# Performance work log

Measured on AMD Instinct MI355X. Metric: run time of the kernel, lower is better.

The kernel has to match this reference:

```python
import jax, jax.numpy as jnp
import numpy as np

B, C, H, W = 2, 256, 64, 64
HEADS, SR = 8, 4
D = C // HEADS          # head dim = 32
N = H * W               # query length = 4096
EPS = 1e-5


def _conv(x, w, stride=1, pad=0, groups=1, b=None):
    out = jax.lax.conv_general_dilated(
        x, w, (stride, stride), [(pad, pad), (pad, pad)],
        dimension_numbers=('NCHW', 'OIHW', 'NCHW'),
        feature_group_count=groups)
    if b is not None:
        out = out + b[None, :, None, None]
    return out


def _bn(x, p):
    # p: [4, C] = (gamma, beta, running_mean, running_var), eval-mode BN
    g, b, m, v = p[0], p[1], p[2], p[3]
    s = g / jnp.sqrt(v + EPS)
    return (x - m[None, :, None, None]) * s[None, :, None, None] + b[None, :, None, None]


def setup_inputs() -> dict:
    key = jax.random.key(0)
    ks = iter(jax.random.split(key, 32))
    nrm = lambda shape, s=0.05: jax.random.normal(next(ks), shape, jnp.float32) * s
    def bnp():
        return jnp.stack([jnp.ones((C,), jnp.float32), jnp.zeros((C,), jnp.float32),
                          jax.random.normal(next(ks), (C,), jnp.float32) * 0.1,
                          jax.random.uniform(next(ks), (C,), jnp.float32) + 0.5])
    return dict(
        x=jax.random.normal(next(ks), (B, C, H, W), jnp.float32),
        relative_pos_enc=jax.random.normal(next(ks), (B, 2, 64, 64), jnp.float32),
        q_w=nrm((C, C, 1, 1)), q_b=jnp.zeros((C,), jnp.float32),
        kv_w=nrm((2 * C, C, 1, 1)), kv_b=jnp.zeros((2 * C,), jnp.float32),
        sr1_dw_w=nrm((C, 1, SR + 3, SR + 3)), sr1_bn1=bnp(),
        sr1_pw_w=nrm((C, 1, 1, 1), 0.5), sr1_bn2=bnp(),
        sr2_dw_w=nrm((C, 1, SR // 2 + 3, SR // 2 + 3)), sr2_bn1=bnp(),
        sr2_pw_w=nrm((C, 1, 1, 1), 0.5), sr2_bn2=bnp(),
        local_w=nrm((C, 1, 3, 3)), local_b=jnp.zeros((C,), jnp.float32),
    )


def reference(x, relative_pos_enc, q_w, q_b, kv_w, kv_b,
              sr1_dw_w, sr1_bn1, sr1_pw_w, sr1_bn2,
              sr2_dw_w, sr2_bn1, sr2_pw_w, sr2_bn2,
              local_w, local_b):
    scale = D ** -0.5
    # q: 1x1 conv -> [B, heads, N, D]; both branches use the FIRST half of heads
    q = _conv(x, q_w, b=q_b).reshape(B, HEADS, D, N).transpose(0, 1, 3, 2)
    qh = q[:, :HEADS // 2]

    def branch(dw_w, bn1, pw_w, bn2, stride, pad, rpe_slice):
        # SR path: depthwise conv + BN + ReLU, depthwise 1x1 + BN
        y = jax.nn.relu(_bn(_conv(x, dw_w, stride, pad, groups=C), bn1))
        y = _bn(_conv(y, pw_w, groups=C), bn2)
        # local 3x3 depthwise mixing with residual
        y = _conv(y, local_w, pad=1, groups=C, b=local_b) + y
        kv = _conv(y, kv_w, b=kv_b)                # [B, 2C, h', w']
        k, v = jnp.split(kv, 2, axis=1)
        L = 2 * y.shape[2] * y.shape[3]            # channel-fold doubles kv length
        k = k.reshape(B, HEADS // 2, D, L)
        v = v.reshape(B, HEADS // 2, D, L).transpose(0, 1, 3, 2)
        attn = jnp.einsum('bhnd,bhdl->bhnl', qh, k) * scale
        rpe = jax.image.resize(rpe_slice, (B, 1, N, L), method='bicubic')
        attn = jax.nn.softmax(attn + rpe, axis=-1)
        return jnp.einsum('bhnl,bhld->bhnd', attn, v)

    x1 = branch(sr1_dw_w, sr1_bn1, sr1_pw_w, sr1_bn2,
                SR, (SR + 3) // 2, relative_pos_enc[:, 0:1])
    x2 = branch(sr2_dw_w, sr2_bn1, sr2_pw_w, sr2_bn2,
                SR // 2, (SR // 2 + 3) // 2, relative_pos_enc[:, 1:2])
    out = jnp.concatenate([x1, x2], axis=-1)       # [B, heads//2, N, 2D]
    return out.reshape(B, C, H, W)
```

## Files before the change

kernel.cpp:

```cpp
#include <hip/hip_runtime.h>
#include <hip/hip_bf16.h>
#include <math.h>

#define NB 2
#define NC 256
#define HWIN 4096
#define NN 4096
#define ND 32
#define NHH 4
#define EPSV 1e-5f

typedef short short8 __attribute__((ext_vector_type(8)));
typedef float f32x4 __attribute__((ext_vector_type(4)));
typedef unsigned short u16;
typedef unsigned int u32;

#define OFF_T1   0
#define OFF_T2   262144
#define OFF_Q    1310720
#define OFF_KT1  1835008
#define OFF_VT1  1900544
#define OFF_KT2  1966080
#define OFF_VT2  2228224
#define OFF_RCT1 2490368
#define OFF_RCT2 2531328
#define OFF_WT   2695168
#define OFF_QWT  5054464
#define OFF_LWP  5087232

#define QSCALE 0.2550437314857726f
#define LOG2E  1.4426950408889634f

__device__ __forceinline__ u16 f2bf(float x) {
  unsigned u = __float_as_uint(x);
  u += 0x7fffu + ((u >> 16) & 1u);
  return (u16)(u >> 16);
}

__device__ __forceinline__ u32 pk_bf16(float a, float b) {
  __hip_bfloat162 h = __float22bfloat162_rn(make_float2(a, b));
  u32 r; __builtin_memcpy(&r, &h, 4);
  return r;
}

__device__ __forceinline__ float keysw(float t) {
  t = fabsf(t);
  float w;
  if (t < 1.f)       w = ((1.5f*t - 2.5f)*t)*t + 1.f;
  else if (t < 2.f)  w = ((-0.5f*t + 2.5f)*t - 4.f)*t + 2.f;
  else               w = 0.f;
  return w;
}

template<int KS, int STR, int PAD, int OH>
__device__ __forceinline__ void dwconv_body(int idx, const float* __restrict__ x,
    const float* __restrict__ dww, const float* __restrict__ bn1,
    const float* __restrict__ pww, const float* __restrict__ bn2,
    float* __restrict__ tout) {
  const int hw = OH*OH;
  int s = idx % hw; int c = (idx/hw) % NC; int b = idx/(hw*NC);
  int oy = s / OH, ox = s % OH;
  const float* xp = x + (b*NC + c)*HWIN;
  const float* wp = dww + c*KS*KS;
  float acc = 0.f;
  #pragma unroll
  for (int ky = 0; ky < KS; ++ky) {
    int iy = oy*STR - PAD + ky;
    if (iy < 0 || iy >= 64) continue;
    #pragma unroll
    for (int kx = 0; kx < KS; ++kx) {
      int ix = ox*STR - PAD + kx;
      if (ix < 0 || ix >= 64) continue;
      acc += xp[iy*64 + ix] * wp[ky*KS + kx];
    }
  }
  float s1 = bn1[c] * rsqrtf(bn1[3*NC + c] + EPSV);
  float z = (acc - bn1[2*NC + c])*s1 + bn1[NC + c];
  z = fmaxf(z, 0.f);
  float s2 = bn2[c] * rsqrtf(bn2[3*NC + c] + EPSV);
  z = z * (pww[c]*s2) + (bn2[NC + c] - bn2[2*NC + c]*s2);
  tout[((size_t)(b*hw + s))*NC + c] = z;
}

__device__ __forceinline__ void rpe_body(int idx, const float* __restrict__ rpe,
                                         u16* __restrict__ rcT, int L, int ch) {
  int r = idx & 63; int l = (idx >> 6) % L; int b = idx / (64*L);
  float f = ((float)l + 0.5f)*(64.f/(float)L) - 0.5f;
  int i0 = (int)floorf(f) - 1;
  const float* rp = rpe + ((b*2 + ch)*64 + r)*64;
  float v = 0.f, wsum = 0.f;
  #pragma unroll
  for (int j = 0; j < 4; ++j) {
    int i = i0 + j;
    if (i >= 0 && i < 64) {
      float w = keysw(f - (float)i);
      v += w * rp[i]; wsum += w;
    }
  }
  rcT[((size_t)(b*L + l))*80 + 4 + r] = f2bf(v / wsum);
}

__global__ void __launch_bounds__(256) prep_kernel(
    const float* __restrict__ x,
    const float* __restrict__ dw1, const float* __restrict__ bn11,
    const float* __restrict__ pw1, const float* __restrict__ bn12, float* __restrict__ t1,
    const float* __restrict__ dw2, const float* __restrict__ bn21,
    const float* __restrict__ pw2, const float* __restrict__ bn22, float* __restrict__ t2,
    const float* __restrict__ rpe, u16* __restrict__ rct1, u16* __restrict__ rct2,
    const float* __restrict__ kvw, float* __restrict__ wtp,
    const float* __restrict__ qw, float* __restrict__ qwp2,
    const float* __restrict__ lw, float* __restrict__ lwp) {
  int blk = blockIdx.x;
  int t = threadIdx.x;
  if (blk < 512) {
    dwconv_body<7,4,3,16>(blk*256 + t, x, dw1, bn11, pw1, bn12, t1);
  } else if (blk < 2560) {
    dwconv_body<5,2,2,32>((blk-512)*256 + t, x, dw2, bn21, pw2, bn22, t2);
  } else if (blk < 2816) {
    rpe_body((blk-2560)*256 + t, rpe, rct1, 512, 0);
  } else if (blk < 3840) {
    rpe_body((blk-2816)*256 + t, rpe, rct2, 2048, 1);
  } else if (blk < 3968) {
    int idx = (blk-3840)*256 + t;
    float4 vv = *(const float4*)(kvw + (size_t)idx*4);
    int o = idx >> 6, c4 = idx & 63;
    *(float4*)(wtp + ((size_t)(c4*512 + o))*4) = vv;
  } else if (blk < 4000) {
    int idx = (blk-3968)*256 + t;
    float4 vv = *(const float4*)(qw + (size_t)idx*4);
    int oc = idx >> 6, c0 = (idx & 63)*4;
    int ocq = oc >> 2, r = oc & 3;
    qwp2[((size_t)((c0+0)*32 + ocq))*4 + r] = vv.x;
    qwp2[((size_t)((c0+1)*32 + ocq))*4 + r] = vv.y;
    qwp2[((size_t)((c0+2)*32 + ocq))*4 + r] = vv.z;
    qwp2[((size_t)((c0+3)*32 + ocq))*4 + r] = vv.w;
  } else {
    int c = t;
    #pragma unroll
    for (int tp = 0; tp < 9; ++tp) lwp[tp*256 + c] = lw[c*9 + tp];
  }
}

__global__ void __launch_bounds__(256) localkv_kernel(
    const float* __restrict__ t1T, const float* __restrict__ t2T,
    const float* __restrict__ lwp, const float* __restrict__ lb,
    const float* __restrict__ wtp, const float* __restrict__ kvb,
    u16* __restrict__ kt1, u16* __restrict__ vt1,
    u16* __restrict__ kt2, u16* __restrict__ vt2,
    const float* __restrict__ x, const float* __restrict__ qwp2,
    const float* __restrict__ qb, u16* __restrict__ q) {
  __shared__ float sbuf[128*32];
  int blk = blockIdx.x, tid = threadIdx.x;
  if (blk < 640) {
    int kv = blk & 1, ti = blk >> 1;
    const float* tT; u16 *kT, *vT; int OH, hw, b, s0;
    if (ti < 64) { tT = t1T; kT = kt1; vT = vt1; OH = 16; hw = 256;  b = ti >> 5; s0 = (ti & 31)*8; }
    else { int v2 = ti-64; tT = t2T; kT = kt2; vT = vt2; OH = 32; hw = 1024; b = v2 >> 7; s0 = (v2 & 127)*8; }
    int oy = s0 / OH, ox0 = s0 % OH;
    const float* tb = tT + (size_t)b*hw*NC;
    int cl = tid & 63, spg = tid >> 6;
    int c0 = cl*4;
    f32x4 wt9[9];
    #pragma unroll
    for (int tp = 0; tp < 9; ++tp) wt9[tp] = *(const f32x4*)(lwp + tp*256 + c0);
    f32x4 lb4 = *(const f32x4*)(lb + c0);
    #pragma unroll
    for (int i = 0; i < 2; ++i) {
      int sp = spg*2 + i;
      int ox = ox0 + sp;
      f32x4 a = lb4;
      #pragma unroll
      for (int dy = 0; dy < 3; ++dy) {
        int iy = oy + dy - 1;
        if (iy < 0 || iy >= OH) continue;
        #pragma unroll
        for (int dx = 0; dx < 3; ++dx) {
          int ix = ox + dx - 1;
          if (ix < 0 || ix >= OH) continue;
          f32x4 tv = *(const f32x4*)(tb + (size_t)(iy*OH + ix)*NC + c0);
          a += tv * wt9[dy*3 + dx];
        }
      }
      a += *(const f32x4*)(tb + (size_t)(oy*OH + ox)*NC + c0);
      *(f32x4*)(sbuf + sp*NC + c0) = a;
    }
    __syncthreads();
    int ol = tid & 127, sph = tid >> 7;
    int o0i = kv*256 + ol, o1i = o0i + 128;
    float acc0[4], acc1[4];
    float b0 = kvb[o0i], b1 = kvb[o1i];
    #pragma unroll
    for (int i = 0; i < 4; ++i) { acc0[i] = b0; acc1[i] = b1; }
    #pragma unroll 2
    for (int c4 = 0; c4 < 64; ++c4) {
      f32x4 w0 = *(const f32x4*)(wtp + ((size_t)(c4*512 + o0i))*4);
      f32x4 w1 = *(const f32x4*)(wtp + ((size_t)(c4*512 + o1i))*4);
      #pragma unroll
      for (int i = 0; i < 4; ++i) {
        f32x4 y4 = *(const f32x4*)(sbuf + (sph*4 + i)*NC + c4*4);
        #pragma unroll
        for (int j = 0; j < 4; ++j) { acc0[i] += w0[j]*y4[j]; acc1[i] += w1[j]*y4[j]; }
      }
    }
    int L2 = 2*hw;
    #pragma unroll
    for (int k = 0; k < 2; ++k) {
      const float* ap = k ? acc1 : acc0;
      int oo = ol + k*128;
      int hh = oo >> 6, r = oo & 63, d = r >> 1, e = r & 1;
      if (kv == 0) {
        u16* kp = kT + ((size_t)((b*NHH + hh)*L2 + e*hw + s0 + sph*4))*ND + d;
        #pragma unroll
        for (int j = 0; j < 4; ++j) kp[j*ND] = f2bf(ap[j]);
      } else {
        int l0v = e*hw + s0 + sph*4;
        u16* vp = vT + ((size_t)((b*NHH + hh)*(L2/64) + (l0v >> 6))*ND + d)*64 + (l0v & 63);
        #pragma unroll
        for (int j = 0; j < 4; ++j) vp[j] = f2bf(ap[j]);
      }
    }
  } else {
    int qblk = blk - 640;
    int b = qblk >> 7;
    int n0 = (qblk & 127) * 32;
    const float* xb = x + (size_t)b*NC*HWIN + n0;
    int ocq = tid & 31, spg = tid >> 5;
    float acc[4][4];
    #pragma unroll
    for (int k = 0; k < 4; ++k) {
      float bias = qb[ocq*4 + k];
      #pragma unroll
      for (int i = 0; i < 4; ++i) acc[k][i] = bias;
    }
    #pragma unroll
    for (int half = 0; half < 2; ++half) {
      #pragma unroll
      for (int j = 0; j < 4; ++j) {
        int u = tid + 256*j;
        int c = u >> 3, spq = u & 7;
        *(f32x4*)(sbuf + c*32 + spq*4) =
            *(const f32x4*)(xb + (size_t)(half*128 + c)*HWIN + spq*4);
      }
      __syncthreads();
      #pragma unroll 4
      for (int c = 0; c < 128; ++c) {
        int cg = half*128 + c;
        f32x4 w4 = *(const f32x4*)(qwp2 + ((size_t)(cg*32 + ocq))*4);
        f32x4 y4 = *(const f32x4*)(sbuf + c*32 + spg*4);
        #pragma unroll
        for (int k = 0; k < 4; ++k)
          #pragma unroll
          for (int i = 0; i < 4; ++i) acc[k][i] += w4[k]*y4[i];
      }
      __syncthreads();
    }
    #pragma unroll
    for (int k = 0; k < 4; ++k) {
      int oc = ocq*4 + k;
      int h = oc >> 5, d = oc & 31;
      u16* qp = q + (((size_t)(b*NHH + h))*NN + n0 + spg*4)*ND + d;
      #pragma unroll
      for (int i = 0; i < 4; ++i) qp[i*ND] = f2bf(acc[k][i]*QSCALE);
    }
  }
}

__global__ void __launch_bounds__(256) attn_kernel(
    const u16* __restrict__ qbf,
    const u16* __restrict__ kt1, const u16* __restrict__ vt1, const u16* __restrict__ rct1,
    const u16* __restrict__ kt2, const u16* __restrict__ vt2, const u16* __restrict__ rct2,
    float* __restrict__ out) {
  __shared__ u16 kbuf[64*32];
  __shared__ u16 vbuf[32*64];
  __shared__ u32 pbuf_all[4][16*32];
  int u = blockIdx.x;
  int br, b, hh, rb;
  if (u < 512) { br = 1; b = u >> 8; hh = (u >> 6) & 3; rb = u & 63; }
  else { int v = u - 512; br = 0; b = v >> 8; hh = (v >> 6) & 3; rb = v & 63; }
  int L = br ? 2048 : 512;
  int nt = br ? 32 : 8;
  const u16* kT  = br ? kt2 : kt1;
  const u16* vT  = br ? vt2 : vt1;
  const u16* rcT = br ? rct2 : rct1;
  int tid = threadIdx.x;
  int w = tid >> 6, lane = tid & 63;
  int g = lane >> 4, lo = lane & 15;
  u32* pbuf = pbuf_all[w];
  u16* pbuf16 = (u16*)pbuf;
  int n = rb*64 + w*16 + lo;

  const u16* kbase = kT + (size_t)(b*NHH + hh)*L*ND;
  const u16* vbase = vT + (size_t)(b*NHH + hh)*ND*L;
  const u16* rcTb  = rcT + (size_t)b*L*80;

  short8 qf = *(const short8*)(qbf + (((size_t)(b*NHH + hh))*NN + n)*ND + 8*g);

  float fr = ((float)n + 0.5f)*(1.f/64.f) - 0.5f;
  int ri0 = (int)floorf(fr) - 1;
  int a = (w < 2) ? rb - 2 : rb - 1;
  int rmin = a & ~3;
  float wr4[4]; float wsum = 0.f;
  #pragma unroll
  for (int j = 0; j < 4; ++j) {
    int i = ri0 + j;
    float wv = (i >= 0 && i < 64) ? keysw(fr - (float)i) : 0.f;
    wr4[j] = wv; wsum += wv;
  }
  float invw = LOG2E / wsum;
  float wt8[8];
  #pragma unroll
  for (int s = 0; s < 8; ++s) {
    float acc = 0.f;
    #pragma unroll
    for (int j = 0; j < 4; ++j)
      acc += (ri0 + j - rmin == s) ? wr4[j]*invw : 0.f;
    wt8[s] = acc;
  }
  short8 wtf;
  {
    u32 p0 = pk_bf16(wt8[0], wt8[1]), p1 = pk_bf16(wt8[2], wt8[3]);
    u32 p2 = pk_bf16(wt8[4], wt8[5]), p3 = pk_bf16(wt8[6], wt8[7]);
    uint4 uu = make_uint4(p0, p1, p2, p3);
    wtf = __builtin_bit_cast(short8, uu);
    if (g != 0) wtf = (short8)0;
  }
  const u16* rcrow0 = rcTb + (rmin + 4);

  const f32x4 zero = {0.f, 0.f, 0.f, 0.f};
  float ssum = 0.f;
  f32x4 o0 = zero, o1 = zero;

  int kr_row = tid >> 2, kr_col = (tid & 3)*8;
  int kr_sw  = ((kr_row >> 1) & 3)*8;
  int vr_row = tid >> 3, vr_col = (tid & 7)*8;
  int vr_sw  = (vr_row & 7)*8;
  int ksw = ((lo >> 1) & 3)*8;
  int vsw = (lo & 7)*8;
  int psw4 = (lo & 7)*4;
  int psw8 = (lo & 7)*8;

  auto stageLoad = [&](short8& kr, short8& vr, int l0) {
    kr = *(const short8*)(kbase + (size_t)(l0 + kr_row)*ND + kr_col);
    vr = *(const short8*)(vbase + (size_t)(l0 >> 6)*(ND*64) + vr_row*64 + vr_col);
  };
  auto stageStore = [&](short8 kr, short8 vr) {
    *(short8*)(kbuf + kr_row*32 + (kr_col ^ kr_sw)) = kr;
    *(short8*)(vbuf + vr_row*64 + (vr_col ^ vr_sw)) = vr;
  };
  auto loadRC = [&](uint4 (&rc)[4], int l0) {
    #pragma unroll
    for (int c = 0; c < 4; ++c) {
      const u16* arow = rcrow0 + (size_t)(l0 + 16*c + lo)*80;
      uint2 ra = *(const uint2*)arow;
      uint2 rb2 = *(const uint2*)(arow + 4);
      rc[c] = make_uint4(ra.x, ra.y, rb2.x, rb2.y);
    }
  };

  short8 kr, vr;
  uint4 rcA[4], rcB[4];
  stageLoad(kr, vr, 0);
  loadRC(rcA, 0);

  for (int t = 0; t < nt; ++t) {
    stageStore(kr, vr);
    __syncthreads();
    if (t < nt-1) { stageLoad(kr, vr, (t+1)*64); loadRC(rcB, (t+1)*64); }
    f32x4 s4[4];
    #pragma unroll
    for (int c = 0; c < 4; ++c) {
      short8 rcf = __builtin_bit_cast(short8, rcA[c]);
      f32x4 accr = __builtin_amdgcn_mfma_f32_16x16x32_bf16(rcf, wtf, zero, 0, 0, 0);
      short8 kf = *(const short8*)(kbuf + (16*c + lo)*32 + ((8*g) ^ ksw));
      s4[c] = __builtin_amdgcn_mfma_f32_16x16x32_bf16(kf, qf, accr, 0, 0, 0);
    }
    float psum = 0.f;
    u32 pk[8];
    #pragma unroll
    for (int c = 0; c < 4; ++c) {
      float p0 = __builtin_amdgcn_exp2f(s4[c][0]);
      float p1 = __builtin_amdgcn_exp2f(s4[c][1]);
      float p2 = __builtin_amdgcn_exp2f(s4[c][2]);
      float p3 = __builtin_amdgcn_exp2f(s4[c][3]);
      psum += (p0 + p1) + (p2 + p3);
      pk[2*c]   = pk_bf16(p0, p1);
      pk[2*c+1] = pk_bf16(p2, p3);
    }
    ssum += psum;
    #pragma unroll
    for (int c = 0; c < 4; ++c)
      *(uint2*)(pbuf + lo*32 + ((8*c + 2*g) ^ psw4)) = make_uint2(pk[2*c], pk[2*c+1]);
    short8 pf0 = *(const short8*)(pbuf16 + lo*64 + ((8*g) ^ psw8));
    short8 pf1 = *(const short8*)(pbuf16 + lo*64 + ((32 + 8*g) ^ psw8));
    short8 v00 = *(const short8*)(vbuf + lo*64 + ((8*g) ^ vsw));
    short8 v01 = *(const short8*)(vbuf + lo*64 + ((32 + 8*g) ^ vsw));
    short8 v10 = *(const short8*)(vbuf + (16 + lo)*64 + ((8*g) ^ vsw));
    short8 v11 = *(const short8*)(vbuf + (16 + lo)*64 + ((32 + 8*g) ^ vsw));
    o0 = __builtin_amdgcn_mfma_f32_16x16x32_bf16(v00, pf0, o0, 0, 0, 0);
    o1 = __builtin_amdgcn_mfma_f32_16x16x32_bf16(v10, pf0, o1, 0, 0, 0);
    o0 = __builtin_amdgcn_mfma_f32_16x16x32_bf16(v01, pf1, o0, 0, 0, 0);
    o1 = __builtin_amdgcn_mfma_f32_16x16x32_bf16(v11, pf1, o1, 0, 0, 0);
    if (t < nt-1) {
      #pragma unroll
      for (int j = 0; j < 4; ++j) rcA[j] = rcB[j];
    }
    __syncthreads();
  }

  ssum += __shfl_xor(ssum, 16, 64);
  ssum += __shfl_xor(ssum, 32, 64);
  float inv = 1.f/ssum;
  f32x4 w0 = o0*inv, w1 = o1*inv;
  float* op = out + ((size_t)((b*NC + hh*64 + rb)*64 + (w*16 + lo)))*64 + (br ? 32 : 0);
  *(f32x4*)(op + 4*g)      = w0;
  *(f32x4*)(op + 16 + 4*g) = w1;
}

extern "C" void kernel_launch(void* const* d_in, const int* in_sizes, int n_in,
                              void* d_out, int out_size, void* d_ws, size_t ws_size,
                              hipStream_t stream) {
  const float* x    = (const float*)d_in[0];
  const float* rpe  = (const float*)d_in[1];
  const float* qw   = (const float*)d_in[2];
  const float* qb   = (const float*)d_in[3];
  const float* kvw  = (const float*)d_in[4];
  const float* kvb  = (const float*)d_in[5];
  const float* dw1  = (const float*)d_in[6];
  const float* bn11 = (const float*)d_in[7];
  const float* pw1  = (const float*)d_in[8];
  const float* bn12 = (const float*)d_in[9];
  const float* dw2  = (const float*)d_in[10];
  const float* bn21 = (const float*)d_in[11];
  const float* pw2  = (const float*)d_in[12];
  const float* bn22 = (const float*)d_in[13];
  const float* lw   = (const float*)d_in[14];
  const float* lb   = (const float*)d_in[15];
  float* out = (float*)d_out;
  float* ws  = (float*)d_ws;

  float* t1   = ws + OFF_T1;
  float* t2   = ws + OFF_T2;
  u16*   q    = (u16*)(ws + OFF_Q);
  u16*   kt1  = (u16*)(ws + OFF_KT1);
  u16*   vt1  = (u16*)(ws + OFF_VT1);
  u16*   kt2  = (u16*)(ws + OFF_KT2);
  u16*   vt2  = (u16*)(ws + OFF_VT2);
  u16*   rct1 = (u16*)(ws + OFF_RCT1);
  u16*   rct2 = (u16*)(ws + OFF_RCT2);
  float* wtp  = ws + OFF_WT;
  float* qwp2 = ws + OFF_QWT;
  float* lwp  = ws + OFF_LWP;

  hipLaunchKernelGGL(prep_kernel, dim3(4001), dim3(256), 0, stream,
                     x, dw1, bn11, pw1, bn12, t1, dw2, bn21, pw2, bn22, t2,
                     rpe, rct1, rct2, kvw, wtp, qw, qwp2, lw, lwp);
  hipLaunchKernelGGL(localkv_kernel, dim3(896), dim3(256), 0, stream,
                     t1, t2, lwp, lb, wtp, kvb, kt1, vt1, kt2, vt2, x, qwp2, qb, q);
  hipLaunchKernelGGL(attn_kernel, dim3(1024), dim3(256), 0, stream,
                     q, kt1, vt1, rct1, kt2, vt2, rct2, out);
}
```

Measured before the change: 171.3 us.

## Merge both attention branches per block and move RPE resize into localkv kernel

The attention kernel now has each block process both branches in sequence (the short L=512 pass, then the L=2048 pass), halving the grid to 512 blocks and reusing the Q fragment and bicubic row weights across the two passes. The RPE bicubic resize work moves from the prep kernel into the localkv kernel as extra blocks, rebalancing work across stages. The intent is to remove the load imbalance between short and long branch blocks and duplicated per-block setup. The risk is fewer blocks in attention, giving lower occupancy and longer serial blocks on a GPU with many CUs.

```diff
diff --git a/kernel.cpp b/kernel.cpp
--- a/kernel.cpp
+++ b/kernel.cpp
@@ -106,7 +106,6 @@
     const float* __restrict__ pw1, const float* __restrict__ bn12, float* __restrict__ t1,
     const float* __restrict__ dw2, const float* __restrict__ bn21,
     const float* __restrict__ pw2, const float* __restrict__ bn22, float* __restrict__ t2,
-    const float* __restrict__ rpe, u16* __restrict__ rct1, u16* __restrict__ rct2,
     const float* __restrict__ kvw, float* __restrict__ wtp,
     const float* __restrict__ qw, float* __restrict__ qwp2,
     const float* __restrict__ lw, float* __restrict__ lwp) {
@@ -116,17 +115,13 @@
     dwconv_body<7,4,3,16>(blk*256 + t, x, dw1, bn11, pw1, bn12, t1);
   } else if (blk < 2560) {
     dwconv_body<5,2,2,32>((blk-512)*256 + t, x, dw2, bn21, pw2, bn22, t2);
-  } else if (blk < 2816) {
-    rpe_body((blk-2560)*256 + t, rpe, rct1, 512, 0);
-  } else if (blk < 3840) {
-    rpe_body((blk-2816)*256 + t, rpe, rct2, 2048, 1);
-  } else if (blk < 3968) {
-    int idx = (blk-3840)*256 + t;
+  } else if (blk < 2688) {
+    int idx = (blk-2560)*256 + t;
     float4 vv = *(const float4*)(kvw + (size_t)idx*4);
     int o = idx >> 6, c4 = idx & 63;
     *(float4*)(wtp + ((size_t)(c4*512 + o))*4) = vv;
-  } else if (blk < 4000) {
-    int idx = (blk-3968)*256 + t;
+  } else if (blk < 2720) {
+    int idx = (blk-2688)*256 + t;
     float4 vv = *(const float4*)(qw + (size_t)idx*4);
     int oc = idx >> 6, c0 = (idx & 63)*4;
     int ocq = oc >> 2, r = oc & 3;
@@ -148,7 +143,8 @@
     u16* __restrict__ kt1, u16* __restrict__ vt1,
     u16* __restrict__ kt2, u16* __restrict__ vt2,
     const float* __restrict__ x, const float* __restrict__ qwp2,
-    const float* __restrict__ qb, u16* __restrict__ q) {
+    const float* __restrict__ qb, u16* __restrict__ q,
+    const float* __restrict__ rpe, u16* __restrict__ rct1, u16* __restrict__ rct2) {
   __shared__ float sbuf[128*32];
   int blk = blockIdx.x, tid = threadIdx.x;
   if (blk < 640) {
@@ -219,7 +215,7 @@
         for (int j = 0; j < 4; ++j) vp[j] = f2bf(ap[j]);
       }
     }
-  } else {
+  } else if (blk < 896) {
     int qblk = blk - 640;
     int b = qblk >> 7;
     int n0 = (qblk & 127) * 32;
@@ -262,6 +258,10 @@
       #pragma unroll
       for (int i = 0; i < 4; ++i) qp[i*ND] = f2bf(acc[k][i]*QSCALE);
     }
+  } else if (blk < 1152) {
+    rpe_body((blk-896)*256 + tid, rpe, rct1, 512, 0);
+  } else {
+    rpe_body((blk-1152)*256 + tid, rpe, rct2, 2048, 1);
   }
 }
 
@@ -274,24 +274,13 @@
   __shared__ u16 vbuf[32*64];
   __shared__ u32 pbuf_all[4][16*32];
   int u = blockIdx.x;
-  int br, b, hh, rb;
-  if (u < 512) { br = 1; b = u >> 8; hh = (u >> 6) & 3; rb = u & 63; }
-  else { int v = u - 512; br = 0; b = v >> 8; hh = (v >> 6) & 3; rb = v & 63; }
-  int L = br ? 2048 : 512;
-  int nt = br ? 32 : 8;
-  const u16* kT  = br ? kt2 : kt1;
-  const u16* vT  = br ? vt2 : vt1;
-  const u16* rcT = br ? rct2 : rct1;
+  int b = u >> 8, hh = (u >> 6) & 3, rb = u & 63;
   int tid = threadIdx.x;
   int w = tid >> 6, lane = tid & 63;
   int g = lane >> 4, lo = lane & 15;
   u32* pbuf = pbuf_all[w];
   u16* pbuf16 = (u16*)pbuf;
   int n = rb*64 + w*16 + lo;
-
-  const u16* kbase = kT + (size_t)(b*NHH + hh)*L*ND;
-  const u16* vbase = vT + (size_t)(b*NHH + hh)*ND*L;
-  const u16* rcTb  = rcT + (size_t)b*L*80;
 
   short8 qf = *(const short8*)(qbf + (((size_t)(b*NHH + hh))*NN + n)*ND + 8*g);
 
@@ -324,11 +313,8 @@
     wtf = __builtin_bit_cast(short8, uu);
     if (g != 0) wtf = (short8)0;
   }
-  const u16* rcrow0 = rcTb + (rmin + 4);
 
   const f32x4 zero = {0.f, 0.f, 0.f, 0.f};
-  float ssum = 0.f;
-  f32x4 o0 = zero, o1 = zero;
 
   int kr_row = tid >> 2, kr_col = (tid & 3)*8;
   int kr_sw  = ((kr_row >> 1) & 3)*8;
@@ -339,81 +325,91 @@
   int psw4 = (lo & 7)*4;
   int psw8 = (lo & 7)*8;
 
-  auto stageLoad = [&](short8& kr, short8& vr, int l0) {
-    kr = *(const short8*)(kbase + (size_t)(l0 + kr_row)*ND + kr_col);
-    vr = *(const short8*)(vbase + (size_t)(l0 >> 6)*(ND*64) + vr_row*64 + vr_col);
-  };
-  auto stageStore = [&](short8 kr, short8 vr) {
-    *(short8*)(kbuf + kr_row*32 + (kr_col ^ kr_sw)) = kr;
-    *(short8*)(vbuf + vr_row*64 + (vr_col ^ vr_sw)) = vr;
-  };
-  auto loadRC = [&](uint4 (&rc)[4], int l0) {
-    #pragma unroll
-    for (int c = 0; c < 4; ++c) {
-      const u16* arow = rcrow0 + (size_t)(l0 + 16*c + lo)*80;
-      uint2 ra = *(const uint2*)arow;
-      uint2 rb2 = *(const uint2*)(arow + 4);
-      rc[c] = make_uint4(ra.x, ra.y, rb2.x, rb2.y);
-    }
-  };
-
-  short8 kr, vr;
-  uint4 rcA[4], rcB[4];
-  stageLoad(kr, vr, 0);
-  loadRC(rcA, 0);
-
-  for (int t = 0; t < nt; ++t) {
-    stageStore(kr, vr);
-    __syncthreads();
-    if (t < nt-1) { stageLoad(kr, vr, (t+1)*64); loadRC(rcB, (t+1)*64); }
-    f32x4 s4[4];
-    #pragma unroll
-    for (int c = 0; c < 4; ++c) {
-      short8 rcf = __builtin_bit_cast(short8, rcA[c]);
-      f32x4 accr = __builtin_amdgcn_mfma_f32_16x16x32_bf16(rcf, wtf, zero, 0, 0, 0);
-      short8 kf = *(const short8*)(kbuf + (16*c + lo)*32 + ((8*g) ^ ksw));
-      s4[c] = __builtin_amdgcn_mfma_f32_16x16x32_bf16(kf, qf, accr, 0, 0, 0);
-    }
-    float psum = 0.f;
-    u32 pk[8];
-    #pragma unroll
-    for (int c = 0; c < 4; ++c) {
-      float p0 = __builtin_amdgcn_exp2f(s4[c][0]);
-      float p1 = __builtin_amdgcn_exp2f(s4[c][1]);
-      float p2 = __builtin_amdgcn_exp2f(s4[c][2]);
-      float p3 = __builtin_amdgcn_exp2f(s4[c][3]);
-      psum += (p0 + p1) + (p2 + p3);
-      pk[2*c]   = pk_bf16(p0, p1);
-      pk[2*c+1] = pk_bf16(p2, p3);
-    }
-    ssum += psum;
-    #pragma unroll
-    for (int c = 0; c < 4; ++c)
-      *(uint2*)(pbuf + lo*32 + ((8*c + 2*g) ^ psw4)) = make_uint2(pk[2*c], pk[2*c+1]);
-    short8 pf0 = *(const short8*)(pbuf16 + lo*64 + ((8*g) ^ psw8));
-    short8 pf1 = *(const short8*)(pbuf16 + lo*64 + ((32 + 8*g) ^ psw8));
-    short8 v00 = *(const short8*)(vbuf + lo*64 + ((8*g) ^ vsw));
-    short8 v01 = *(const short8*)(vbuf + lo*64 + ((32 + 8*g) ^ vsw));
-    short8 v10 = *(const short8*)(vbuf + (16 + lo)*64 + ((8*g) ^ vsw));
-    short8 v11 = *(const short8*)(vbuf + (16 + lo)*64 + ((32 + 8*g) ^ vsw));
-    o0 = __builtin_amdgcn_mfma_f32_16x16x32_bf16(v00, pf0, o0, 0, 0, 0);
-    o1 = __builtin_amdgcn_mfma_f32_16x16x32_bf16(v10, pf0, o1, 0, 0, 0);
-    o0 = __builtin_amdgcn_mfma_f32_16x16x32_bf16(v01, pf1, o0, 0, 0, 0);
-    o1 = __builtin_amdgcn_mfma_f32_16x16x32_bf16(v11, pf1, o1, 0, 0, 0);
-    if (t < nt-1) {
-      #pragma unroll
-      for (int j = 0; j < 4; ++j) rcA[j] = rcB[j];
-    }
-    __syncthreads();
-  }
-
-  ssum += __shfl_xor(ssum, 16, 64);
-  ssum += __shfl_xor(ssum, 32, 64);
-  float inv = 1.f/ssum;
-  f32x4 w0 = o0*inv, w1 = o1*inv;
-  float* op = out + ((size_t)((b*NC + hh*64 + rb)*64 + (w*16 + lo)))*64 + (br ? 32 : 0);
-  *(f32x4*)(op + 4*g)      = w0;
-  *(f32x4*)(op + 16 + 4*g) = w1;
+  for (int pass = 0; pass < 2; ++pass) {
+    const int L  = pass ? 2048 : 512;
+    const int nt = pass ? 32 : 8;
+    const u16* kbase  = (pass ? kt2 : kt1) + (size_t)(b*NHH + hh)*L*ND;
+    const u16* vbase  = (pass ? vt2 : vt1) + (size_t)(b*NHH + hh)*ND*L;
+    const u16* rcrow0 = (pass ? rct2 : rct1) + (size_t)b*L*80 + (rmin + 4);
+
+    auto stageLoad = [&](short8& kr, short8& vr, int l0) {
+      kr = *(const short8*)(kbase + (size_t)(l0 + kr_row)*ND + kr_col);
+      vr = *(const short8*)(vbase + (size_t)(l0 >> 6)*(ND*64) + vr_row*64 + vr_col);
+    };
+    auto stageStore = [&](short8 kr, short8 vr) {
+      *(short8*)(kbuf + kr_row*32 + (kr_col ^ kr_sw)) = kr;
+      *(short8*)(vbuf + vr_row*64 + (vr_col ^ vr_sw)) = vr;
+    };
+    auto loadRC = [&](uint4 (&rc)[4], int l0) {
+      #pragma unroll
+      for (int c = 0; c < 4; ++c) {
+        const u16* arow = rcrow0 + (size_t)(l0 + 16*c + lo)*80;
+        uint2 ra = *(const uint2*)arow;
+        uint2 rb2 = *(const uint2*)(arow + 4);
+        rc[c] = make_uint4(ra.x, ra.y, rb2.x, rb2.y);
+      }
+    };
+
+    float ssum = 0.f;
+    f32x4 o0 = zero, o1 = zero;
+    short8 kr, vr;
+    uint4 rcA[4], rcB[4];
+    stageLoad(kr, vr, 0);
+    loadRC(rcA, 0);
+
+    for (int t = 0; t < nt; ++t) {
+      stageStore(kr, vr);
+      __syncthreads();
+      if (t < nt-1) { stageLoad(kr, vr, (t+1)*64); loadRC(rcB, (t+1)*64); }
+      f32x4 s4[4];
+      #pragma unroll
+      for (int c = 0; c < 4; ++c) {
+        short8 rcf = __builtin_bit_cast(short8, rcA[c]);
+        f32x4 accr = __builtin_amdgcn_mfma_f32_16x16x32_bf16(rcf, wtf, zero, 0, 0, 0);
+        short8 kf = *(const short8*)(kbuf + (16*c + lo)*32 + ((8*g) ^ ksw));
+        s4[c] = __builtin_amdgcn_mfma_f32_16x16x32_bf16(kf, qf, accr, 0, 0, 0);
+      }
+      float psum = 0.f;
+      u32 pk[8];
+      #pragma unroll
+      for (int c = 0; c < 4; ++c) {
+        float p0 = __builtin_amdgcn_exp2f(s4[c][0]);
+        float p1 = __builtin_amdgcn_exp2f(s4[c][1]);
+        float p2 = __builtin_amdgcn_exp2f(s4[c][2]);
+        float p3 = __builtin_amdgcn_exp2f(s4[c][3]);
+        psum += (p0 + p1) + (p2 + p3);
+        pk[2*c]   = pk_bf16(p0, p1);
+        pk[2*c+1] = pk_bf16(p2, p3);
+      }
+      ssum += psum;
+      #pragma unroll
+      for (int c = 0; c < 4; ++c)
+        *(uint2*)(pbuf + lo*32 + ((8*c + 2*g) ^ psw4)) = make_uint2(pk[2*c], pk[2*c+1]);
+      short8 pf0 = *(const short8*)(pbuf16 + lo*64 + ((8*g) ^ psw8));
+      short8 pf1 = *(const short8*)(pbuf16 + lo*64 + ((32 + 8*g) ^ psw8));
+      short8 v00 = *(const short8*)(vbuf + lo*64 + ((8*g) ^ vsw));
+      short8 v01 = *(const short8*)(vbuf + lo*64 + ((32 + 8*g) ^ vsw));
+      short8 v10 = *(const short8*)(vbuf + (16 + lo)*64 + ((8*g) ^ vsw));
+      short8 v11 = *(const short8*)(vbuf + (16 + lo)*64 + ((32 + 8*g) ^ vsw));
+      o0 = __builtin_amdgcn_mfma_f32_16x16x32_bf16(v00, pf0, o0, 0, 0, 0);
+      o1 = __builtin_amdgcn_mfma_f32_16x16x32_bf16(v10, pf0, o1, 0, 0, 0);
+      o0 = __builtin_amdgcn_mfma_f32_16x16x32_bf16(v01, pf1, o0, 0, 0, 0);
+      o1 = __builtin_amdgcn_mfma_f32_16x16x32_bf16(v11, pf1, o1, 0, 0, 0);
+      if (t < nt-1) {
+        #pragma unroll
+        for (int j = 0; j < 4; ++j) rcA[j] = rcB[j];
+      }
+      __syncthreads();
+    }
+
+    ssum += __shfl_xor(ssum, 16, 64);
+    ssum += __shfl_xor(ssum, 32, 64);
+    float inv = 1.f/ssum;
+    f32x4 w0 = o0*inv, w1 = o1*inv;
+    float* op = out + ((size_t)((b*NC + hh*64 + rb)*64 + (w*16 + lo)))*64 + pass*32;
+    *(f32x4*)(op + 4*g)      = w0;
+    *(f32x4*)(op + 16 + 4*g) = w1;
+  }
 }
 
 extern "C" void kernel_launch(void* const* d_in, const int* in_sizes, int n_in,
@@ -451,11 +447,12 @@
   float* qwp2 = ws + OFF_QWT;
   float* lwp  = ws + OFF_LWP;
 
-  hipLaunchKernelGGL(prep_kernel, dim3(4001), dim3(256), 0, stream,
+  hipLaunchKernelGGL(prep_kernel, dim3(2721), dim3(256), 0, stream,
                      x, dw1, bn11, pw1, bn12, t1, dw2, bn21, pw2, bn22, t2,
-                     rpe, rct1, rct2, kvw, wtp, qw, qwp2, lw, lwp);
-  hipLaunchKernelGGL(localkv_kernel, dim3(896), dim3(256), 0, stream,
-                     t1, t2, lwp, lb, wtp, kvb, kt1, vt1, kt2, vt2, x, qwp2, qb, q);
-  hipLaunchKernelGGL(attn_kernel, dim3(1024), dim3(256), 0, stream,
+                     kvw, wtp, qw, qwp2, lw, lwp);
+  hipLaunchKernelGGL(localkv_kernel, dim3(2176), dim3(256), 0, stream,
+                     t1, t2, lwp, lb, wtp, kvb, kt1, vt1, kt2, vt2, x, qwp2, qb, q,
+                     rpe, rct1, rct2);
+  hipLaunchKernelGGL(attn_kernel, dim3(512), dim3(256), 0, stream,
                      q, kt1, vt1, rct1, kt2, vt2, rct2, out);
 }
```

Measured after the change: 180.5 us. 1.05x slower.

## Load K/V fragments directly from global into registers, drop LDS staging and barriers

Applied to the files above, without the earlier changes.

The attention kernel stops staging K and V tiles through shared memory. Each wave now loads its MFMA fragments straight from global memory into registers, double-buffered across two tiles. This removes the LDS stores and both block-wide __syncthreads per tile, and adds s_setprio around the compute. Launch bounds now request 3 blocks per CU. The cost is that every wave loads K/V redundantly (four times more global/L2 traffic), plus higher register pressure from holding two tiles of fragments.

```diff
diff --git a/kernel.cpp b/kernel.cpp
--- a/kernel.cpp
+++ b/kernel.cpp
@@ -265,13 +265,11 @@
   }
 }
 
-__global__ void __launch_bounds__(256) attn_kernel(
+__global__ void __launch_bounds__(256, 3) attn_kernel(
     const u16* __restrict__ qbf,
     const u16* __restrict__ kt1, const u16* __restrict__ vt1, const u16* __restrict__ rct1,
     const u16* __restrict__ kt2, const u16* __restrict__ vt2, const u16* __restrict__ rct2,
     float* __restrict__ out) {
-  __shared__ u16 kbuf[64*32];
-  __shared__ u16 vbuf[32*64];
   __shared__ u32 pbuf_all[4][16*32];
   int u = blockIdx.x;
   int br, b, hh, rb;
@@ -330,22 +328,20 @@
   float ssum = 0.f;
   f32x4 o0 = zero, o1 = zero;
 
-  int kr_row = tid >> 2, kr_col = (tid & 3)*8;
-  int kr_sw  = ((kr_row >> 1) & 3)*8;
-  int vr_row = tid >> 3, vr_col = (tid & 7)*8;
-  int vr_sw  = (vr_row & 7)*8;
-  int ksw = ((lo >> 1) & 3)*8;
-  int vsw = (lo & 7)*8;
   int psw4 = (lo & 7)*4;
   int psw8 = (lo & 7)*8;
 
-  auto stageLoad = [&](short8& kr, short8& vr, int l0) {
-    kr = *(const short8*)(kbase + (size_t)(l0 + kr_row)*ND + kr_col);
-    vr = *(const short8*)(vbase + (size_t)(l0 >> 6)*(ND*64) + vr_row*64 + vr_col);
+  auto loadK = [&](short8 (&kf)[4], int l0) {
+    #pragma unroll
+    for (int c = 0; c < 4; ++c)
+      kf[c] = *(const short8*)(kbase + (size_t)(l0 + 16*c + lo)*ND + 8*g);
   };
-  auto stageStore = [&](short8 kr, short8 vr) {
-    *(short8*)(kbuf + kr_row*32 + (kr_col ^ kr_sw)) = kr;
-    *(short8*)(vbuf + vr_row*64 + (vr_col ^ vr_sw)) = vr;
+  auto loadV = [&](short8 (&vf)[4], int l0) {
+    const u16* vt = vbase + (size_t)(l0 >> 6)*(ND*64);
+    vf[0] = *(const short8*)(vt + lo*64 + 8*g);
+    vf[1] = *(const short8*)(vt + lo*64 + 32 + 8*g);
+    vf[2] = *(const short8*)(vt + (16 + lo)*64 + 8*g);
+    vf[3] = *(const short8*)(vt + (16 + lo)*64 + 32 + 8*g);
   };
   auto loadRC = [&](uint4 (&rc)[4], int l0) {
     #pragma unroll
@@ -357,22 +353,14 @@
     }
   };
 
-  short8 kr, vr;
-  uint4 rcA[4], rcB[4];
-  stageLoad(kr, vr, 0);
-  loadRC(rcA, 0);
-
-  for (int t = 0; t < nt; ++t) {
-    stageStore(kr, vr);
-    __syncthreads();
-    if (t < nt-1) { stageLoad(kr, vr, (t+1)*64); loadRC(rcB, (t+1)*64); }
+  auto computeTile = [&](short8 (&kf)[4], short8 (&vf)[4], uint4 (&rc)[4]) {
+    __builtin_amdgcn_s_setprio(1);
     f32x4 s4[4];
     #pragma unroll
     for (int c = 0; c < 4; ++c) {
-      short8 rcf = __builtin_bit_cast(short8, rcA[c]);
+      short8 rcf = __builtin_bit_cast(short8, rc[c]);
       f32x4 accr = __builtin_amdgcn_mfma_f32_16x16x32_bf16(rcf, wtf, zero, 0, 0, 0);
-      short8 kf = *(const short8*)(kbuf + (16*c + lo)*32 + ((8*g) ^ ksw));
-      s4[c] = __builtin_amdgcn_mfma_f32_16x16x32_bf16(kf, qf, accr, 0, 0, 0);
+      s4[c] = __builtin_amdgcn_mfma_f32_16x16x32_bf16(kf[c], qf, accr, 0, 0, 0);
     }
     float psum = 0.f;
     u32 pk[8];
@@ -392,19 +380,22 @@
       *(uint2*)(pbuf + lo*32 + ((8*c + 2*g) ^ psw4)) = make_uint2(pk[2*c], pk[2*c+1]);
     short8 pf0 = *(const short8*)(pbuf16 + lo*64 + ((8*g) ^ psw8));
     short8 pf1 = *(const short8*)(pbuf16 + lo*64 + ((32 + 8*g) ^ psw8));
-    short8 v00 = *(const short8*)(vbuf + lo*64 + ((8*g) ^ vsw));
-    short8 v01 = *(const short8*)(vbuf + lo*64 + ((32 + 8*g) ^ vsw));
-    short8 v10 = *(const short8*)(vbuf + (16 + lo)*64 + ((8*g) ^ vsw));
-    short8 v11 = *(const short8*)(vbuf + (16 + lo)*64 + ((32 + 8*g) ^ vsw));
-    o0 = __builtin_amdgcn_mfma_f32_16x16x32_bf16(v00, pf0, o0, 0, 0, 0);
-    o1 = __builtin_amdgcn_mfma_f32_16x16x32_bf16(v10, pf0, o1, 0, 0, 0);
-    o0 = __builtin_amdgcn_mfma_f32_16x16x32_bf16(v01, pf1, o0, 0, 0, 0);
-    o1 = __builtin_amdgcn_mfma_f32_16x16x32_bf16(v11, pf1, o1, 0, 0, 0);
-    if (t < nt-1) {
-      #pragma unroll
-      for (int j = 0; j < 4; ++j) rcA[j] = rcB[j];
-    }
-    __syncthreads();
+    o0 = __builtin_amdgcn_mfma_f32_16x16x32_bf16(vf[0], pf0, o0, 0, 0, 0);
+    o1 = __builtin_amdgcn_mfma_f32_16x16x32_bf16(vf[2], pf0, o1, 0, 0, 0);
+    o0 = __builtin_amdgcn_mfma_f32_16x16x32_bf16(vf[1], pf1, o0, 0, 0, 0);
+    o1 = __builtin_amdgcn_mfma_f32_16x16x32_bf16(vf[3], pf1, o1, 0, 0, 0);
+    __builtin_amdgcn_s_setprio(0);
+  };
+
+  short8 kfA[4], vfA[4], kfB[4], vfB[4];
+  uint4 rcA[4], rcB[4];
+  loadK(kfA, 0); loadV(vfA, 0); loadRC(rcA, 0);
+
+  for (int t = 0; t < nt; t += 2) {
+    if (t + 1 < nt) { loadK(kfB, (t+1)*64); loadV(vfB, (t+1)*64); loadRC(rcB, (t+1)*64); }
+    computeTile(kfA, vfA, rcA);
+    if (t + 2 < nt) { loadK(kfA, (t+2)*64); loadV(vfA, (t+2)*64); loadRC(rcA, (t+2)*64); }
+    if (t + 1 < nt) computeTile(kfB, vfB, rcB);
   }
 
   ssum += __shfl_xor(ssum, 16, 64);
```

Result: slower. 209.9 us (+22.5%).
